# Kernel optimization log

Measured on AMD Instinct MI355X. Metric: run time of the kernel, lower is better.

Reference implementation:

```python
import jax, jax.numpy as jnp
import numpy as np

D = 32        # dmodel (forced by reshape(..., 32) in the original)
N = 2000      # n_nodes == liner_fourth
SLOPE = 0.2   # LeakyReLU negative slope
EPS = 1e-6    # SublayerConnection LayerNorm eps (annotated-transformer style)


def _layernorm(x, g, b):
    m = x.mean(-1, keepdims=True)
    v = x.var(-1, keepdims=True)
    return g * (x - m) / jnp.sqrt(v + EPS) + b


def setup_inputs() -> dict:
    key = jax.random.key(0)
    ks = jax.random.split(key, 18)
    F_, NL, NS = 16, 500, 1500
    s = 0.1
    return {
        "state": jax.random.normal(ks[0], (F_, NS, D), jnp.float32),
        "left": jax.random.normal(ks[1], (F_, NL, D), jnp.float32),
        "inputad": jax.random.bernoulli(ks[2], 0.02, (F_, N, N)).astype(jnp.float32),
        "w3": s * jax.random.normal(ks[3], (D, D), jnp.float32),       # linearThird
        "b3": jnp.zeros((D,), jnp.float32),
        "attn_w": s * jax.random.normal(ks[4], (1, 2 * D), jnp.float32),  # attn (no bias)
        "w4": s * jax.random.normal(ks[5], (D, N), jnp.float32),       # linearFourth: 2000->32
        "b4": jnp.zeros((D,), jnp.float32),
        "w1": s * jax.random.normal(ks[6], (D, D), jnp.float32),       # linear
        "b1": jnp.zeros((D,), jnp.float32),
        "w_ih": s * jax.random.normal(ks[7], (4 * D, D), jnp.float32),  # LSTMCell (gate order i,f,g,o)
        "w_hh": s * jax.random.normal(ks[8], (4 * D, D), jnp.float32),
        "b_ih": jnp.zeros((4 * D,), jnp.float32),
        "b_hh": jnp.zeros((4 * D,), jnp.float32),
        "ln_g": jnp.ones((D,), jnp.float32),                            # SublayerConnection norm
        "ln_b": jnp.zeros((D,), jnp.float32),
        "w2": s * jax.random.normal(ks[9], (D, D), jnp.float32),        # linearSecond
        "b2": jnp.zeros((D,), jnp.float32),
    }


def reference(state, left, inputad, w3, b3, attn_w, w4, b4, w1, b1,
              w_ih, w_hh, b_ih, b_hh, ln_g, ln_b, w2, b2):
    # eval mode: all dropouts are identity
    x = jnp.concatenate([left, state], axis=1)          # [F, N, D]
    F_, n = x.shape[0], x.shape[1]
    g = x @ w3.T + b3                                   # [F, N, D]

    # torch: e = leaky(attn(cat([g.repeat_interleave(n,0), g.repeat(n,1,1)], -1)))
    # Decompose the linear over the concat: attn_w = [a_l | a_r].
    # g_repeat_interleave row m -> g[m // n]; g_repeat row m -> g[m % F_];
    # e.view(F_, n, n)[b, i, j] = e_flat[b*n + i, j].
    a_l, a_r = attn_w[0, :D], attn_w[0, D:]
    s_l = g @ a_l                                        # [F, N]
    s_r = g @ a_r                                        # [F, N]
    idx = (jnp.arange(F_)[:, None] * n + jnp.arange(n)[None, :]) % F_  # [F, N]
    e_mat = jax.nn.leaky_relu(s_l[:, None, :] + s_r[idx], SLOPE)       # [F, N, N]

    e_masked = jnp.where(inputad == 0, 0.0, e_mat)       # masked_fill(adj==0, 0)
    h = jax.nn.leaky_relu(jnp.einsum('bij,oj->bio', e_masked, w4) + b4, SLOPE)  # [F, N, 32]

    # first softmax(e)/dropout pair is dead code (overwritten); a = softmax(h, dim=1)
    a = jax.nn.softmax(h, axis=1)
    st = (a * g) @ w1.T + b1                             # elementwise branch (a.shape == g.shape)

    agg = jnp.matmul(inputad, st)                        # bmm(degree2, state): [F, N, D]

    # SublayerConnection: st + dropout(sublayer(norm(st))); sublayer = LSTMCell cell-state
    nx = _layernorm(st, ln_g, ln_b)
    c0 = nx.reshape(-1, D)                               # initial cell state = norm(st)
    # h0 = zeros, so the w_hh @ h0 contribution vanishes (b_hh still applies)
    gates = agg.reshape(-1, D) @ w_ih.T + b_ih + b_hh    # [F*N, 4D]
    i_g = jax.nn.sigmoid(gates[:, :D])
    f_g = jax.nn.sigmoid(gates[:, D:2 * D])
    g_g = jnp.tanh(gates[:, 2 * D:3 * D])
    c1 = f_g * c0 + i_g * g_g                            # LSTMCell returns (h', c'); [1] -> c'

    out = st + c1.reshape(F_, n, D)
    return out @ w2.T + b2
```

## Files before the change

### kernel.cpp

```cpp
#include <hip/hip_runtime.h>
#include <math.h>

#define F_    16
#define NROW  2000
#define NL    500
#define D     32
#define ROWS  (F_*NROW)
#define SLOPE 0.2f
#define CAP   128
#define LCAP  256

typedef float f4 __attribute__((ext_vector_type(4)));

__global__ __launch_bounds__(256) void k1_g(
    const float* __restrict__ state, const float* __restrict__ left,
    const float* __restrict__ w3, const float* __restrict__ b3,
    const float* __restrict__ attn_w, const float* __restrict__ w4,
    float* __restrict__ g, float* __restrict__ s_l, float* __restrict__ s_r,
    float* __restrict__ w4t)
{
    int bid = blockIdx.x;
    int t = threadIdx.x;
    if (bid >= ROWS/8) {
        int k = (bid - ROWS/8) * 256 + t;
        if (k < D * NROW) {
            int o = k / NROW, j = k - o * NROW;
            w4t[j * D + o] = w4[k];
        }
        return;
    }
    __shared__ float sw3[D*33];
    __shared__ float sb3[D], sal[D], sar[D];
    for (int k = t; k < D*D; k += 256) sw3[(k>>5)*33 + (k&31)] = w3[k];
    if (t < D) { sb3[t] = b3[t]; sal[t] = attn_w[t]; sar[t] = attn_w[D + t]; }
    __syncthreads();
    int grp = t >> 5, lane = t & 31;
    int row = bid * 8 + grp;
    int b = row / NROW, i = row - b * NROW;
    const float* xrow = (i < NL) ? (left  + ((size_t)b * NL + i) * D)
                                 : (state + ((size_t)b * (NROW - NL) + (i - NL)) * D);
    float x = xrow[lane];
    float acc = sb3[lane];
#pragma unroll
    for (int k = 0; k < D; ++k)
        acc += __shfl(x, k, 32) * sw3[lane*33 + k];
    g[(size_t)row * D + lane] = acc;
    float pl = acc * sal[lane], pr = acc * sar[lane];
#pragma unroll
    for (int m = 16; m >= 1; m >>= 1) {
        pl += __shfl_xor(pl, m, 32);
        pr += __shfl_xor(pr, m, 32);
    }
    if (lane == 0) { s_l[row] = pl; s_r[row] = pr; }
}

__global__ __launch_bounds__(256) void k2a_compact(
    const float* __restrict__ adj,
    int* __restrict__ nzc, unsigned short* __restrict__ nzi)
{
    __shared__ unsigned short sh_j[4][LCAP+8];
    int t = threadIdx.x;
    int w = t >> 6, lane = t & 63;
    int row = blockIdx.x * 4 + w;
    const f4* mrow = reinterpret_cast<const f4*>(adj + (size_t)row * NROW);

    f4 v[8];
#pragma unroll
    for (int it = 0; it < 7; ++it)
        v[it] = __builtin_nontemporal_load(mrow + it * 64 + lane);
    v[7] = (f4)(0.f);
    if (448 + lane < NROW/4) v[7] = __builtin_nontemporal_load(mrow + 448 + lane);

    int c = 0;
#pragma unroll
    for (int it = 0; it < 8; ++it)
        c += (v[it][0] != 0.f) + (v[it][1] != 0.f) + (v[it][2] != 0.f) + (v[it][3] != 0.f);
    int inc = c;
#pragma unroll
    for (int off = 1; off < 64; off <<= 1) {
        int n = __shfl_up(inc, off, 64);
        inc += (lane >= off) ? n : 0;
    }
    int pos = inc - c;
    int cnt = __shfl(inc, 63, 64);

#pragma unroll
    for (int it = 0; it < 8; ++it) {
        int jb = (it * 64 + lane) * 4;
#pragma unroll
        for (int cc = 0; cc < 4; ++cc) {
            float val = v[it][cc];
            int hit = (val != 0.f);
            int tgt = (hit && pos < LCAP) ? pos : LCAP;
            sh_j[w][tgt] = (unsigned short)(jb + cc);
            pos += hit;
        }
    }
    int cc2 = (cnt < CAP) ? cnt : CAP;
    for (int k = lane; k < cc2; k += 64)
        nzi[(size_t)row * CAP + k] = sh_j[w][k];
    if (lane == 0) nzc[row] = cc2;
}

__global__ __launch_bounds__(256) void k2b_h(
    const float* __restrict__ s_l, const float* __restrict__ s_r,
    const float* __restrict__ w4t, const float* __restrict__ b4,
    const int* __restrict__ nzc, const unsigned short* __restrict__ nzi,
    float* __restrict__ h)
{
    __shared__ float sh_e[8][CAP];
    __shared__ unsigned short sh_jj[8][CAP];
    int t = threadIdx.x;
    int grp = t >> 5, lane = t & 31;
    int row = blockIdx.x * 8 + grp;
    int b = row / NROW, i = row - b * NROW;
    int r = i & 15;
    int cnt = nzc[row];
    const unsigned short* lst = nzi + (size_t)row * CAP;
    const float* slb = s_l + (size_t)b * NROW;
    const float* srr = s_r + (size_t)r * NROW;
    for (int k = lane; k < cnt; k += 32) {
        int j = lst[k];
        sh_jj[grp][k] = (unsigned short)j;
        float e = slb[j] + srr[j];
        sh_e[grp][k] = (e > 0.f) ? e : SLOPE * e;
    }
    float acc = 0.f;
    int k = 0;
    for (; k + 4 <= cnt; k += 4) {
        int j0 = sh_jj[grp][k],   j1 = sh_jj[grp][k+1];
        int j2 = sh_jj[grp][k+2], j3 = sh_jj[grp][k+3];
        float w0 = w4t[j0*D + lane], w1 = w4t[j1*D + lane];
        float w2v = w4t[j2*D + lane], w3v = w4t[j3*D + lane];
        acc += sh_e[grp][k]   * w0 + sh_e[grp][k+1] * w1
             + sh_e[grp][k+2] * w2v + sh_e[grp][k+3] * w3v;
    }
    for (; k < cnt; ++k)
        acc += sh_e[grp][k] * w4t[sh_jj[grp][k]*D + lane];
    float hv = acc + b4[lane];
    h[(size_t)row * D + lane] = (hv > 0.f) ? hv : SLOPE * hv;
}

__global__ __launch_bounds__(256) void k3a_psum(const float* __restrict__ h,
                                                float* __restrict__ psum)
{
    int b = blockIdx.x, slice = blockIdx.y;
    int t = threadIdx.x;
    int o = t & 31, ti = t >> 5;
    int base = slice * 125;
    float s = 0.f;
    for (int i = base + ti; i < base + 125; i += 8)
        s += expf(h[((size_t)b * NROW + i) * D + o]);
    __shared__ float red[8][D];
    red[ti][o] = s;
    __syncthreads();
    if (t < D) {
        float tot = 0.f;
#pragma unroll
        for (int k = 0; k < 8; ++k) tot += red[k][t];
        psum[((size_t)b * 16 + slice) * D + t] = tot;
    }
}

__global__ __launch_bounds__(256) void k3b_st(
    const float* __restrict__ h, const float* __restrict__ g,
    const float* __restrict__ psum,
    const float* __restrict__ w1, const float* __restrict__ b1,
    float* __restrict__ st)
{
    __shared__ float sw1[D*33], sb1[D], ssum[D];
    int t = threadIdx.x;
    int bid = blockIdx.x;
    int b = bid / 250;
    for (int k = t; k < D*D; k += 256) sw1[(k>>5)*33 + (k&31)] = w1[k];
    if (t < D) {
        sb1[t] = b1[t];
        float tot = 0.f;
#pragma unroll
        for (int s = 0; s < 16; ++s) tot += psum[((size_t)b * 16 + s) * D + t];
        ssum[t] = tot;
    }
    __syncthreads();
    int grp = t >> 5, lane = t & 31;
    size_t row = (size_t)bid * 8 + grp;
    float p = (expf(h[row * D + lane]) / ssum[lane]) * g[row * D + lane];
    float acc = sb1[lane];
#pragma unroll
    for (int k = 0; k < D; ++k)
        acc += __shfl(p, k, 32) * sw1[lane*33 + k];
    st[row * D + lane] = acc;
}

__global__ __launch_bounds__(256) void k4_final(
    const float* __restrict__ st,
    const int* __restrict__ nzc, const unsigned short* __restrict__ nzi,
    const float* __restrict__ w_ih, const float* __restrict__ b_ih,
    const float* __restrict__ b_hh,
    const float* __restrict__ ln_g, const float* __restrict__ ln_b,
    const float* __restrict__ w2, const float* __restrict__ b2,
    float* __restrict__ out)
{
    __shared__ float swih[96*33];
    __shared__ float sw2[D*33];
    __shared__ float sbg[96];
    __shared__ float sb2[D], slg[D], slb[D];
    __shared__ unsigned short jl[8][CAP];
    __shared__ float aggsh[8][D];
    __shared__ float s2sh[8][D];

    int t = threadIdx.x;
    for (int k = t; k < 96*D; k += 256) swih[(k/D)*33 + (k%D)] = w_ih[k];
    for (int k = t; k < D*D;  k += 256) sw2 [(k/D)*33 + (k%D)] = w2[k];
    if (t < 96) sbg[t] = b_ih[t] + b_hh[t];
    if (t < D) { sb2[t] = b2[t]; slg[t] = ln_g[t]; slb[t] = ln_b[t]; }

    int grp = t >> 5, lane = t & 31;
    int row = blockIdx.x * 8 + grp;
    int b = row / NROW;
    int cnt = nzc[row];
    const unsigned short* lst = nzi + (size_t)row * CAP;
    for (int k = lane; k < cnt; k += 32) jl[grp][k] = lst[k];
    __syncthreads();

    const float* stb = st + (size_t)b * NROW * D;
    float agg = 0.f;
    int k = 0;
    for (; k + 8 <= cnt; k += 8) {
        int j0 = jl[grp][k],   j1 = jl[grp][k+1], j2 = jl[grp][k+2], j3 = jl[grp][k+3];
        int j4 = jl[grp][k+4], j5 = jl[grp][k+5], j6 = jl[grp][k+6], j7 = jl[grp][k+7];
        float a0 = stb[j0*D + lane], a1 = stb[j1*D + lane];
        float a2 = stb[j2*D + lane], a3 = stb[j3*D + lane];
        float a4 = stb[j4*D + lane], a5 = stb[j5*D + lane];
        float a6 = stb[j6*D + lane], a7 = stb[j7*D + lane];
        agg += ((a0 + a1) + (a2 + a3)) + ((a4 + a5) + (a6 + a7));
    }
    for (; k < cnt; ++k) agg += stb[jl[grp][k]*D + lane];

    float sv = st[(size_t)row * D + lane];

    float sum = sv;
#pragma unroll
    for (int m = 16; m >= 1; m >>= 1) sum += __shfl_xor(sum, m, 32);
    float mean = sum * (1.f / D);
    float dd = sv - mean;
    float vs = dd * dd;
#pragma unroll
    for (int m = 16; m >= 1; m >>= 1) vs += __shfl_xor(vs, m, 32);
    float inv = 1.f / sqrtf(vs * (1.f / D) + 1e-6f);
    float nx = slg[lane] * dd * inv + slb[lane];

    aggsh[grp][lane] = agg;

    float gi = sbg[lane], gf = sbg[lane + 32], gg = sbg[lane + 64];
#pragma unroll
    for (int d = 0; d < D; ++d) {
        float a = aggsh[grp][d];
        gi += swih[lane*33 + d]      * a;
        gf += swih[(lane+32)*33 + d] * a;
        gg += swih[(lane+64)*33 + d] * a;
    }
    float ig  = 1.f / (1.f + expf(-gi));
    float fg  = 1.f / (1.f + expf(-gf));
    float g_g = tanhf(gg);
    float s2  = sv + fg * nx + ig * g_g;

    s2sh[grp][lane] = s2;

    float acc = sb2[lane];
#pragma unroll
    for (int q = 0; q < D; ++q) acc += sw2[lane*33 + q] * s2sh[grp][q];
    out[(size_t)row * D + lane] = acc;
}

extern "C" void kernel_launch(void* const* d_in, const int* in_sizes, int n_in,
                              void* d_out, int out_size, void* d_ws, size_t ws_size,
                              hipStream_t stream)
{
    const float* state  = (const float*)d_in[0];
    const float* left   = (const float*)d_in[1];
    const float* adj    = (const float*)d_in[2];
    const float* w3     = (const float*)d_in[3];
    const float* b3     = (const float*)d_in[4];
    const float* attn_w = (const float*)d_in[5];
    const float* w4     = (const float*)d_in[6];
    const float* b4     = (const float*)d_in[7];
    const float* w1     = (const float*)d_in[8];
    const float* b1     = (const float*)d_in[9];
    const float* w_ih   = (const float*)d_in[10];
    const float* b_ih   = (const float*)d_in[12];
    const float* b_hh   = (const float*)d_in[13];
    const float* ln_g   = (const float*)d_in[14];
    const float* ln_b   = (const float*)d_in[15];
    const float* w2     = (const float*)d_in[16];
    const float* b2     = (const float*)d_in[17];
    float* out = (float*)d_out;

    float* g    = (float*)d_ws;
    float* h    = g  + (size_t)ROWS * D;
    float* st   = h  + (size_t)ROWS * D;
    float* s_l  = st + (size_t)ROWS * D;
    float* s_r  = s_l + ROWS;
    float* w4t  = s_r + ROWS;
    float* psum = w4t + (size_t)NROW * D;
    int*   nzc  = (int*)(psum + F_ * 16 * D);
    unsigned short* nzi = (unsigned short*)(nzc + ROWS);

    k1_g    <<<dim3(ROWS/8 + (D*NROW+255)/256), dim3(256), 0, stream>>>(
                state, left, w3, b3, attn_w, w4, g, s_l, s_r, w4t);
    k2a_compact<<<dim3(ROWS/4), dim3(256), 0, stream>>>(adj, nzc, nzi);
    k2b_h   <<<dim3(ROWS/8),  dim3(256), 0, stream>>>(s_l, s_r, w4t, b4, nzc, nzi, h);
    k3a_psum<<<dim3(F_, 16),  dim3(256), 0, stream>>>(h, psum);
    k3b_st  <<<dim3(ROWS/8),  dim3(256), 0, stream>>>(h, g, psum, w1, b1, st);
    k4_final<<<dim3(ROWS/8),  dim3(256), 0, stream>>>(st, nzc, nzi, w_ih, b_ih, b_hh,
                                                      ln_g, ln_b, w2, b2, out);
}
```

Before: 132.8 us.

## Fuse six kernels into one persistent kernel with software grid barriers

Replaces the six separate launches with a single persistent kernel of 512 blocks. Each block owns a contiguous slice of rows within one batch, and the phases are separated by atomic-counter grid barriers. The barrier counter is cleared by a memset before the launch. The softmax partial sums are now folded into the h phase, which removes a separate launch. This is meant to remove launch gaps and the small psum kernel, at the cost of having far fewer blocks per phase and relying on every block being co-resident, which could deadlock if not all blocks fit.

```diff
diff --git a/kernel.cpp b/kernel.cpp
--- a/kernel.cpp
+++ b/kernel.cpp
@@ -9,267 +9,266 @@
 #define SLOPE 0.2f
 #define CAP   128
 #define LCAP  256
+#define NBLK  512
+#define TPB   256
 
 typedef float f4 __attribute__((ext_vector_type(4)));
 
-__global__ __launch_bounds__(256) void k1_g(
+struct PA { float sw3[D*33]; float sb3[D]; float sal[D]; float sar[D];
+            unsigned short shj[4][LCAP+8]; };
+struct PB { float red[8][D]; float she[8][CAP]; unsigned short shjj[8][CAP]; };
+struct PC { float sw1[D*33]; float sb1[D]; float ssum[D]; };
+struct PD { float swih[96*33]; float sw2[D*33]; float sbg[96];
+            float sb2[D]; float slg[D]; float slb[D];
+            unsigned short jl[8][CAP]; float aggsh[8][D]; float s2sh[8][D]; };
+union SMU { PA a; PB b; PC c; PD d; };
+
+__device__ __forceinline__ void gridbar(int* bar, int id) {
+    __syncthreads();
+    __threadfence();
+    if (threadIdx.x == 0) {
+        __hip_atomic_fetch_add(bar + id * 32, 1, __ATOMIC_ACQ_REL,
+                               __HIP_MEMORY_SCOPE_AGENT);
+        while (__hip_atomic_load(bar + id * 32, __ATOMIC_ACQUIRE,
+                                 __HIP_MEMORY_SCOPE_AGENT) < NBLK)
+            __builtin_amdgcn_s_sleep(2);
+    }
+    __syncthreads();
+    __threadfence();
+}
+
+__global__ __launch_bounds__(TPB, 2) void mega(
     const float* __restrict__ state, const float* __restrict__ left,
+    const float* __restrict__ adj,
     const float* __restrict__ w3, const float* __restrict__ b3,
     const float* __restrict__ attn_w, const float* __restrict__ w4,
-    float* __restrict__ g, float* __restrict__ s_l, float* __restrict__ s_r,
-    float* __restrict__ w4t)
-{
-    int bid = blockIdx.x;
-    int t = threadIdx.x;
-    if (bid >= ROWS/8) {
-        int k = (bid - ROWS/8) * 256 + t;
-        if (k < D * NROW) {
-            int o = k / NROW, j = k - o * NROW;
-            w4t[j * D + o] = w4[k];
-        }
-        return;
-    }
-    __shared__ float sw3[D*33];
-    __shared__ float sb3[D], sal[D], sar[D];
-    for (int k = t; k < D*D; k += 256) sw3[(k>>5)*33 + (k&31)] = w3[k];
-    if (t < D) { sb3[t] = b3[t]; sal[t] = attn_w[t]; sar[t] = attn_w[D + t]; }
-    __syncthreads();
-    int grp = t >> 5, lane = t & 31;
-    int row = bid * 8 + grp;
-    int b = row / NROW, i = row - b * NROW;
-    const float* xrow = (i < NL) ? (left  + ((size_t)b * NL + i) * D)
-                                 : (state + ((size_t)b * (NROW - NL) + (i - NL)) * D);
-    float x = xrow[lane];
-    float acc = sb3[lane];
-#pragma unroll
-    for (int k = 0; k < D; ++k)
-        acc += __shfl(x, k, 32) * sw3[lane*33 + k];
-    g[(size_t)row * D + lane] = acc;
-    float pl = acc * sal[lane], pr = acc * sar[lane];
-#pragma unroll
-    for (int m = 16; m >= 1; m >>= 1) {
-        pl += __shfl_xor(pl, m, 32);
-        pr += __shfl_xor(pr, m, 32);
-    }
-    if (lane == 0) { s_l[row] = pl; s_r[row] = pr; }
-}
-
-__global__ __launch_bounds__(256) void k2a_compact(
-    const float* __restrict__ adj,
-    int* __restrict__ nzc, unsigned short* __restrict__ nzi)
-{
-    __shared__ unsigned short sh_j[4][LCAP+8];
-    int t = threadIdx.x;
-    int w = t >> 6, lane = t & 63;
-    int row = blockIdx.x * 4 + w;
-    const f4* mrow = reinterpret_cast<const f4*>(adj + (size_t)row * NROW);
-
-    f4 v[8];
-#pragma unroll
-    for (int it = 0; it < 7; ++it)
-        v[it] = __builtin_nontemporal_load(mrow + it * 64 + lane);
-    v[7] = (f4)(0.f);
-    if (448 + lane < NROW/4) v[7] = __builtin_nontemporal_load(mrow + 448 + lane);
-
-    int c = 0;
-#pragma unroll
-    for (int it = 0; it < 8; ++it)
-        c += (v[it][0] != 0.f) + (v[it][1] != 0.f) + (v[it][2] != 0.f) + (v[it][3] != 0.f);
-    int inc = c;
-#pragma unroll
-    for (int off = 1; off < 64; off <<= 1) {
-        int n = __shfl_up(inc, off, 64);
-        inc += (lane >= off) ? n : 0;
-    }
-    int pos = inc - c;
-    int cnt = __shfl(inc, 63, 64);
-
-#pragma unroll
-    for (int it = 0; it < 8; ++it) {
-        int jb = (it * 64 + lane) * 4;
-#pragma unroll
-        for (int cc = 0; cc < 4; ++cc) {
-            float val = v[it][cc];
-            int hit = (val != 0.f);
-            int tgt = (hit && pos < LCAP) ? pos : LCAP;
-            sh_j[w][tgt] = (unsigned short)(jb + cc);
-            pos += hit;
-        }
-    }
-    int cc2 = (cnt < CAP) ? cnt : CAP;
-    for (int k = lane; k < cc2; k += 64)
-        nzi[(size_t)row * CAP + k] = sh_j[w][k];
-    if (lane == 0) nzc[row] = cc2;
-}
-
-__global__ __launch_bounds__(256) void k2b_h(
-    const float* __restrict__ s_l, const float* __restrict__ s_r,
-    const float* __restrict__ w4t, const float* __restrict__ b4,
-    const int* __restrict__ nzc, const unsigned short* __restrict__ nzi,
-    float* __restrict__ h)
-{
-    __shared__ float sh_e[8][CAP];
-    __shared__ unsigned short sh_jj[8][CAP];
-    int t = threadIdx.x;
-    int grp = t >> 5, lane = t & 31;
-    int row = blockIdx.x * 8 + grp;
-    int b = row / NROW, i = row - b * NROW;
-    int r = i & 15;
-    int cnt = nzc[row];
-    const unsigned short* lst = nzi + (size_t)row * CAP;
-    const float* slb = s_l + (size_t)b * NROW;
-    const float* srr = s_r + (size_t)r * NROW;
-    for (int k = lane; k < cnt; k += 32) {
-        int j = lst[k];
-        sh_jj[grp][k] = (unsigned short)j;
-        float e = slb[j] + srr[j];
-        sh_e[grp][k] = (e > 0.f) ? e : SLOPE * e;
-    }
-    float acc = 0.f;
-    int k = 0;
-    for (; k + 4 <= cnt; k += 4) {
-        int j0 = sh_jj[grp][k],   j1 = sh_jj[grp][k+1];
-        int j2 = sh_jj[grp][k+2], j3 = sh_jj[grp][k+3];
-        float w0 = w4t[j0*D + lane], w1 = w4t[j1*D + lane];
-        float w2v = w4t[j2*D + lane], w3v = w4t[j3*D + lane];
-        acc += sh_e[grp][k]   * w0 + sh_e[grp][k+1] * w1
-             + sh_e[grp][k+2] * w2v + sh_e[grp][k+3] * w3v;
-    }
-    for (; k < cnt; ++k)
-        acc += sh_e[grp][k] * w4t[sh_jj[grp][k]*D + lane];
-    float hv = acc + b4[lane];
-    h[(size_t)row * D + lane] = (hv > 0.f) ? hv : SLOPE * hv;
-}
-
-__global__ __launch_bounds__(256) void k3a_psum(const float* __restrict__ h,
-                                                float* __restrict__ psum)
-{
-    int b = blockIdx.x, slice = blockIdx.y;
-    int t = threadIdx.x;
-    int o = t & 31, ti = t >> 5;
-    int base = slice * 125;
-    float s = 0.f;
-    for (int i = base + ti; i < base + 125; i += 8)
-        s += expf(h[((size_t)b * NROW + i) * D + o]);
-    __shared__ float red[8][D];
-    red[ti][o] = s;
-    __syncthreads();
-    if (t < D) {
-        float tot = 0.f;
-#pragma unroll
-        for (int k = 0; k < 8; ++k) tot += red[k][t];
-        psum[((size_t)b * 16 + slice) * D + t] = tot;
-    }
-}
-
-__global__ __launch_bounds__(256) void k3b_st(
-    const float* __restrict__ h, const float* __restrict__ g,
-    const float* __restrict__ psum,
+    const float* __restrict__ b4,
     const float* __restrict__ w1, const float* __restrict__ b1,
-    float* __restrict__ st)
-{
-    __shared__ float sw1[D*33], sb1[D], ssum[D];
-    int t = threadIdx.x;
-    int bid = blockIdx.x;
-    int b = bid / 250;
-    for (int k = t; k < D*D; k += 256) sw1[(k>>5)*33 + (k&31)] = w1[k];
-    if (t < D) {
-        sb1[t] = b1[t];
-        float tot = 0.f;
-#pragma unroll
-        for (int s = 0; s < 16; ++s) tot += psum[((size_t)b * 16 + s) * D + t];
-        ssum[t] = tot;
-    }
-    __syncthreads();
-    int grp = t >> 5, lane = t & 31;
-    size_t row = (size_t)bid * 8 + grp;
-    float p = (expf(h[row * D + lane]) / ssum[lane]) * g[row * D + lane];
-    float acc = sb1[lane];
-#pragma unroll
-    for (int k = 0; k < D; ++k)
-        acc += __shfl(p, k, 32) * sw1[lane*33 + k];
-    st[row * D + lane] = acc;
-}
-
-__global__ __launch_bounds__(256) void k4_final(
-    const float* __restrict__ st,
-    const int* __restrict__ nzc, const unsigned short* __restrict__ nzi,
     const float* __restrict__ w_ih, const float* __restrict__ b_ih,
     const float* __restrict__ b_hh,
     const float* __restrict__ ln_g, const float* __restrict__ ln_b,
     const float* __restrict__ w2, const float* __restrict__ b2,
-    float* __restrict__ out)
+    float* __restrict__ out,
+    int* bar, float* g, float* h, float* st, float* s_l, float* s_r,
+    float* w4t, float* psum, int* nzc, unsigned short* nzi)
 {
-    __shared__ float swih[96*33];
-    __shared__ float sw2[D*33];
-    __shared__ float sbg[96];
-    __shared__ float sb2[D], slg[D], slb[D];
-    __shared__ unsigned short jl[8][CAP];
-    __shared__ float aggsh[8][D];
-    __shared__ float s2sh[8][D];
-
+    __shared__ SMU sm;
+    int q = blockIdx.x;
     int t = threadIdx.x;
-    for (int k = t; k < 96*D; k += 256) swih[(k/D)*33 + (k%D)] = w_ih[k];
-    for (int k = t; k < D*D;  k += 256) sw2 [(k/D)*33 + (k%D)] = w2[k];
-    if (t < 96) sbg[t] = b_ih[t] + b_hh[t];
-    if (t < D) { sb2[t] = b2[t]; slg[t] = ln_g[t]; slb[t] = ln_b[t]; }
-
     int grp = t >> 5, lane = t & 31;
-    int row = blockIdx.x * 8 + grp;
-    int b = row / NROW;
-    int cnt = nzc[row];
-    const unsigned short* lst = nzi + (size_t)row * CAP;
-    for (int k = lane; k < cnt; k += 32) jl[grp][k] = lst[k];
+    int wv = t >> 6, lane64 = t & 63;
+
+    int b  = q >> 5, ss = q & 31;
+    int lo = (ss < 16) ? ss * 63 : 16 * 63 + (ss - 16) * 62;
+    int n  = (ss < 16) ? 63 : 62;
+    int rowbase = b * NROW + lo;
+
+    for (int k = t; k < D*D; k += TPB) sm.a.sw3[(k>>5)*33 + (k&31)] = w3[k];
+    if (t < D) { sm.a.sb3[t] = b3[t]; sm.a.sal[t] = attn_w[t]; sm.a.sar[t] = attn_w[D+t]; }
+    __syncthreads();
+
+    for (int it = 0; it < 8; ++it) {
+        int r = it * 8 + grp;
+        if (r < n) {
+            int row = rowbase + r;
+            int i = lo + r;
+            const float* xrow = (i < NL) ? (left  + ((size_t)b * NL + i) * D)
+                                         : (state + ((size_t)b * (NROW-NL) + (i-NL)) * D);
+            float x = xrow[lane];
+            float acc = sm.a.sb3[lane];
+#pragma unroll
+            for (int k = 0; k < D; ++k)
+                acc += __shfl(x, k, 32) * sm.a.sw3[lane*33 + k];
+            g[(size_t)row * D + lane] = acc;
+            float pl = acc * sm.a.sal[lane], pr = acc * sm.a.sar[lane];
+#pragma unroll
+            for (int m = 16; m >= 1; m >>= 1) {
+                pl += __shfl_xor(pl, m, 32);
+                pr += __shfl_xor(pr, m, 32);
+            }
+            if (lane == 0) { s_l[row] = pl; s_r[row] = pr; }
+        }
+    }
+
+    { int k = q * TPB + t;
+      if (k < D * NROW) { int o = k / NROW, j = k - o * NROW; w4t[j*D + o] = w4[k]; } }
+
+    unsigned long long lmask = (1ull << lane64) - 1ull;
+    for (int rr = wv; rr < n; rr += 4) {
+        int row = rowbase + rr;
+        const f4* mrow = reinterpret_cast<const f4*>(adj + (size_t)row * NROW);
+        f4 v[8];
+#pragma unroll
+        for (int it = 0; it < 7; ++it)
+            v[it] = __builtin_nontemporal_load(mrow + it * 64 + lane64);
+        v[7] = (f4)(0.f);
+        if (448 + lane64 < NROW/4) v[7] = __builtin_nontemporal_load(mrow + 448 + lane64);
+
+        int c = 0;
+#pragma unroll
+        for (int it = 0; it < 8; ++it)
+            c += (v[it][0]!=0.f) + (v[it][1]!=0.f) + (v[it][2]!=0.f) + (v[it][3]!=0.f);
+        int inc = c;
+#pragma unroll
+        for (int off = 1; off < 64; off <<= 1) {
+            int nn = __shfl_up(inc, off, 64);
+            inc += (lane64 >= off) ? nn : 0;
+        }
+        int pos = inc - c;
+        int cnt = __shfl(inc, 63, 64);
+#pragma unroll
+        for (int it = 0; it < 8; ++it) {
+            int jb = (it * 64 + lane64) * 4;
+#pragma unroll
+            for (int cc = 0; cc < 4; ++cc) {
+                int hit = (v[it][cc] != 0.f);
+                int tgt = (hit && pos < LCAP) ? pos : LCAP;
+                sm.a.shj[wv][tgt] = (unsigned short)(jb + cc);
+                pos += hit;
+            }
+        }
+        int cc2 = (cnt < CAP) ? cnt : CAP;
+        for (int k = lane64; k < cc2; k += 64)
+            nzi[(size_t)row * CAP + k] = sm.a.shj[wv][k];
+        if (lane64 == 0) nzc[row] = cc2;
+    }
+
+    gridbar(bar, 0);
+
+    float esum = 0.f;
+    for (int it = 0; it < 8; ++it) {
+        int r = it * 8 + grp;
+        if (r < n) {
+            int row = rowbase + r;
+            int i = lo + r;
+            int cnt = nzc[row];
+            const unsigned short* lst = nzi + (size_t)row * CAP;
+            const float* slb = s_l + (size_t)b * NROW;
+            const float* srr = s_r + (size_t)(i & 15) * NROW;
+            for (int k = lane; k < cnt; k += 32) {
+                int j = lst[k];
+                sm.b.shjj[grp][k] = (unsigned short)j;
+                float e = slb[j] + srr[j];
+                sm.b.she[grp][k] = (e > 0.f) ? e : SLOPE * e;
+            }
+            float acc = 0.f;
+            int k = 0;
+            for (; k + 4 <= cnt; k += 4) {
+                int j0 = sm.b.shjj[grp][k],   j1 = sm.b.shjj[grp][k+1];
+                int j2 = sm.b.shjj[grp][k+2], j3 = sm.b.shjj[grp][k+3];
+                acc += sm.b.she[grp][k]   * w4t[j0*D + lane]
+                     + sm.b.she[grp][k+1] * w4t[j1*D + lane]
+                     + sm.b.she[grp][k+2] * w4t[j2*D + lane]
+                     + sm.b.she[grp][k+3] * w4t[j3*D + lane];
+            }
+            for (; k < cnt; ++k)
+                acc += sm.b.she[grp][k] * w4t[sm.b.shjj[grp][k]*D + lane];
+            float hv = acc + b4[lane];
+            hv = (hv > 0.f) ? hv : SLOPE * hv;
+            h[(size_t)row * D + lane] = hv;
+            esum += expf(hv);
+        }
+    }
+    sm.b.red[grp][lane] = esum;
+    __syncthreads();
+    if (t < D) {
+        float tot = 0.f;
+#pragma unroll
+        for (int k = 0; k < 8; ++k) tot += sm.b.red[k][t];
+        psum[q * D + t] = tot;
+    }
+
+    gridbar(bar, 1);
+
+    for (int k = t; k < D*D; k += TPB) sm.c.sw1[(k>>5)*33 + (k&31)] = w1[k];
+    if (t < D) {
+        sm.c.sb1[t] = b1[t];
+        float tot = 0.f;
+#pragma unroll
+        for (int s = 0; s < 32; ++s) tot += psum[(b * 32 + s) * D + t];
+        sm.c.ssum[t] = tot;
+    }
+    __syncthreads();
+    for (int it = 0; it < 8; ++it) {
+        int r = it * 8 + grp;
+        if (r < n) {
+            size_t row = (size_t)rowbase + r;
+            float p = (expf(h[row*D + lane]) / sm.c.ssum[lane]) * g[row*D + lane];
+            float acc = sm.c.sb1[lane];
+#pragma unroll
+            for (int k = 0; k < D; ++k)
+                acc += __shfl(p, k, 32) * sm.c.sw1[lane*33 + k];
+            st[row*D + lane] = acc;
+        }
+    }
+
+    gridbar(bar, 2);
+
+    for (int k = t; k < 96*D; k += TPB) sm.d.swih[(k/D)*33 + (k%D)] = w_ih[k];
+    for (int k = t; k < D*D;  k += TPB) sm.d.sw2 [(k/D)*33 + (k%D)] = w2[k];
+    if (t < 96) sm.d.sbg[t] = b_ih[t] + b_hh[t];
+    if (t < D) { sm.d.sb2[t] = b2[t]; sm.d.slg[t] = ln_g[t]; sm.d.slb[t] = ln_b[t]; }
     __syncthreads();
 
     const float* stb = st + (size_t)b * NROW * D;
-    float agg = 0.f;
-    int k = 0;
-    for (; k + 8 <= cnt; k += 8) {
-        int j0 = jl[grp][k],   j1 = jl[grp][k+1], j2 = jl[grp][k+2], j3 = jl[grp][k+3];
-        int j4 = jl[grp][k+4], j5 = jl[grp][k+5], j6 = jl[grp][k+6], j7 = jl[grp][k+7];
-        float a0 = stb[j0*D + lane], a1 = stb[j1*D + lane];
-        float a2 = stb[j2*D + lane], a3 = stb[j3*D + lane];
-        float a4 = stb[j4*D + lane], a5 = stb[j5*D + lane];
-        float a6 = stb[j6*D + lane], a7 = stb[j7*D + lane];
-        agg += ((a0 + a1) + (a2 + a3)) + ((a4 + a5) + (a6 + a7));
-    }
-    for (; k < cnt; ++k) agg += stb[jl[grp][k]*D + lane];
-
-    float sv = st[(size_t)row * D + lane];
-
-    float sum = sv;
-#pragma unroll
-    for (int m = 16; m >= 1; m >>= 1) sum += __shfl_xor(sum, m, 32);
-    float mean = sum * (1.f / D);
-    float dd = sv - mean;
-    float vs = dd * dd;
-#pragma unroll
-    for (int m = 16; m >= 1; m >>= 1) vs += __shfl_xor(vs, m, 32);
-    float inv = 1.f / sqrtf(vs * (1.f / D) + 1e-6f);
-    float nx = slg[lane] * dd * inv + slb[lane];
-
-    aggsh[grp][lane] = agg;
-
-    float gi = sbg[lane], gf = sbg[lane + 32], gg = sbg[lane + 64];
-#pragma unroll
-    for (int d = 0; d < D; ++d) {
-        float a = aggsh[grp][d];
-        gi += swih[lane*33 + d]      * a;
-        gf += swih[(lane+32)*33 + d] * a;
-        gg += swih[(lane+64)*33 + d] * a;
-    }
-    float ig  = 1.f / (1.f + expf(-gi));
-    float fg  = 1.f / (1.f + expf(-gf));
-    float g_g = tanhf(gg);
-    float s2  = sv + fg * nx + ig * g_g;
-
-    s2sh[grp][lane] = s2;
-
-    float acc = sb2[lane];
-#pragma unroll
-    for (int q = 0; q < D; ++q) acc += sw2[lane*33 + q] * s2sh[grp][q];
-    out[(size_t)row * D + lane] = acc;
+    for (int it = 0; it < 8; ++it) {
+        int r = it * 8 + grp;
+        if (r < n) {
+            int row = rowbase + r;
+            int cnt = nzc[row];
+            const unsigned short* lst = nzi + (size_t)row * CAP;
+            for (int k = lane; k < cnt; k += 32) sm.d.jl[grp][k] = lst[k];
+
+            float agg = 0.f;
+            int k = 0;
+            for (; k + 8 <= cnt; k += 8) {
+                int j0 = sm.d.jl[grp][k],   j1 = sm.d.jl[grp][k+1];
+                int j2 = sm.d.jl[grp][k+2], j3 = sm.d.jl[grp][k+3];
+                int j4 = sm.d.jl[grp][k+4], j5 = sm.d.jl[grp][k+5];
+                int j6 = sm.d.jl[grp][k+6], j7 = sm.d.jl[grp][k+7];
+                float a0 = stb[j0*D + lane], a1 = stb[j1*D + lane];
+                float a2 = stb[j2*D + lane], a3 = stb[j3*D + lane];
+                float a4 = stb[j4*D + lane], a5 = stb[j5*D + lane];
+                float a6 = stb[j6*D + lane], a7 = stb[j7*D + lane];
+                agg += ((a0+a1) + (a2+a3)) + ((a4+a5) + (a6+a7));
+            }
+            for (; k < cnt; ++k) agg += stb[sm.d.jl[grp][k]*D + lane];
+
+            float sv = st[(size_t)row * D + lane];
+            float sum = sv;
+#pragma unroll
+            for (int m = 16; m >= 1; m >>= 1) sum += __shfl_xor(sum, m, 32);
+            float mean = sum * (1.f / D);
+            float dd = sv - mean;
+            float vs = dd * dd;
+#pragma unroll
+            for (int m = 16; m >= 1; m >>= 1) vs += __shfl_xor(vs, m, 32);
+            float inv = 1.f / sqrtf(vs * (1.f / D) + 1e-6f);
+            float nx = sm.d.slg[lane] * dd * inv + sm.d.slb[lane];
+
+            sm.d.aggsh[grp][lane] = agg;
+
+            float gi = sm.d.sbg[lane], gf = sm.d.sbg[lane+32], gg = sm.d.sbg[lane+64];
+#pragma unroll
+            for (int d = 0; d < D; ++d) {
+                float a = sm.d.aggsh[grp][d];
+                gi += sm.d.swih[lane*33 + d]      * a;
+                gf += sm.d.swih[(lane+32)*33 + d] * a;
+                gg += sm.d.swih[(lane+64)*33 + d] * a;
+            }
+            float ig  = 1.f / (1.f + expf(-gi));
+            float fg  = 1.f / (1.f + expf(-gf));
+            float g_g = tanhf(gg);
+            float s2  = sv + fg * nx + ig * g_g;
+
+            sm.d.s2sh[grp][lane] = s2;
+
+            float acc = sm.d.sb2[lane];
+#pragma unroll
+            for (int qq = 0; qq < D; ++qq) acc += sm.d.sw2[lane*33 + qq] * sm.d.s2sh[grp][qq];
+            out[(size_t)row * D + lane] = acc;
+        }
+    }
 }
 
 extern "C" void kernel_launch(void* const* d_in, const int* in_sizes, int n_in,
@@ -295,22 +294,20 @@
     const float* b2     = (const float*)d_in[17];
     float* out = (float*)d_out;
 
-    float* g    = (float*)d_ws;
+    int*   bar  = (int*)d_ws;
+    float* g    = (float*)((char*)d_ws + 1024);
     float* h    = g  + (size_t)ROWS * D;
     float* st   = h  + (size_t)ROWS * D;
     float* s_l  = st + (size_t)ROWS * D;
     float* s_r  = s_l + ROWS;
     float* w4t  = s_r + ROWS;
     float* psum = w4t + (size_t)NROW * D;
-    int*   nzc  = (int*)(psum + F_ * 16 * D);
+    int*   nzc  = (int*)(psum + NBLK * D);
     unsigned short* nzi = (unsigned short*)(nzc + ROWS);
 
-    k1_g    <<<dim3(ROWS/8 + (D*NROW+255)/256), dim3(256), 0, stream>>>(
-                state, left, w3, b3, attn_w, w4, g, s_l, s_r, w4t);
-    k2a_compact<<<dim3(ROWS/4), dim3(256), 0, stream>>>(adj, nzc, nzi);
-    k2b_h   <<<dim3(ROWS/8),  dim3(256), 0, stream>>>(s_l, s_r, w4t, b4, nzc, nzi, h);
-    k3a_psum<<<dim3(F_, 16),  dim3(256), 0, stream>>>(h, psum);
-    k3b_st  <<<dim3(ROWS/8),  dim3(256), 0, stream>>>(h, g, psum, w1, b1, st);
-    k4_final<<<dim3(ROWS/8),  dim3(256), 0, stream>>>(st, nzc, nzi, w_ih, b_ih, b_hh,
-                                                      ln_g, ln_b, w2, b2, out);
+    hipMemsetAsync(bar, 0, 1024, stream);
+    mega<<<dim3(NBLK), dim3(TPB), 0, stream>>>(
+        state, left, adj, w3, b3, attn_w, w4, b4, w1, b1,
+        w_ih, b_ih, b_hh, ln_g, ln_b, w2, b2, out,
+        bar, g, h, st, s_l, s_r, w4t, psum, nzc, nzi);
 }
```

Result: slower. 521.5 us (+292.9%).

## Flatten adjacency compaction into grid-stride stream with atomics; fuse softmax sums

Applied to the files above, without the earlier changes.

Replaces the one-row-per-wave compaction of the dense adjacency with a flat grid-stride stream over the whole matrix. Each wave builds per-row prefix sums from ballots and reserves slots with atomicAdd on per-row counters, which are zeroed by a memset. The per-column exp-sum for the softmax is folded into the h kernel through atomic adds, which removes the separate partial-sum kernel. Neighbour order and summation order become nondeterministic, and each step now pays for atomics and scattered narrow stores.

```diff
diff --git a/kernel.cpp b/kernel.cpp
--- a/kernel.cpp
+++ b/kernel.cpp
@@ -8,7 +8,9 @@
 #define ROWS  (F_*NROW)
 #define SLOPE 0.2f
 #define CAP   128
-#define LCAP  256
+#define NF4   (ROWS*NROW/4)
+#define SBLK  2048
+#define STRD  (SBLK*256)
 
 typedef float f4 __attribute__((ext_vector_type(4)));
 
@@ -54,68 +56,65 @@
     if (lane == 0) { s_l[row] = pl; s_r[row] = pr; }
 }
 
-__global__ __launch_bounds__(256) void k2a_compact(
+__global__ __launch_bounds__(256) void k2a_flat(
     const float* __restrict__ adj,
     int* __restrict__ nzc, unsigned short* __restrict__ nzi)
 {
-    __shared__ unsigned short sh_j[4][LCAP+8];
-    int t = threadIdx.x;
-    int w = t >> 6, lane = t & 63;
-    int row = blockIdx.x * 4 + w;
-    const f4* mrow = reinterpret_cast<const f4*>(adj + (size_t)row * NROW);
-
-    f4 v[8];
-#pragma unroll
-    for (int it = 0; it < 7; ++it)
-        v[it] = __builtin_nontemporal_load(mrow + it * 64 + lane);
-    v[7] = (f4)(0.f);
-    if (448 + lane < NROW/4) v[7] = __builtin_nontemporal_load(mrow + 448 + lane);
-
-    int c = 0;
-#pragma unroll
-    for (int it = 0; it < 8; ++it)
-        c += (v[it][0] != 0.f) + (v[it][1] != 0.f) + (v[it][2] != 0.f) + (v[it][3] != 0.f);
-    int inc = c;
-#pragma unroll
-    for (int off = 1; off < 64; off <<= 1) {
-        int n = __shfl_up(inc, off, 64);
-        inc += (lane >= off) ? n : 0;
-    }
-    int pos = inc - c;
-    int cnt = __shfl(inc, 63, 64);
-
-#pragma unroll
-    for (int it = 0; it < 8; ++it) {
-        int jb = (it * 64 + lane) * 4;
-#pragma unroll
-        for (int cc = 0; cc < 4; ++cc) {
-            float val = v[it][cc];
-            int hit = (val != 0.f);
-            int tgt = (hit && pos < LCAP) ? pos : LCAP;
-            sh_j[w][tgt] = (unsigned short)(jb + cc);
-            pos += hit;
-        }
-    }
-    int cc2 = (cnt < CAP) ? cnt : CAP;
-    for (int k = lane; k < cc2; k += 64)
-        nzi[(size_t)row * CAP + k] = sh_j[w][k];
-    if (lane == 0) nzc[row] = cc2;
+    const f4* adj4 = reinterpret_cast<const f4*>(adj);
+    int tid = blockIdx.x * 256 + threadIdx.x;
+    int lane = threadIdx.x & 63;
+    unsigned long long lmask = (1ull << lane) - 1ull;
+
+    for (int idx = tid; idx < NF4; idx += STRD) {
+        f4 v = adj4[idx];
+        int row = idx / 500;
+        int jb  = (idx - row * 500) * 4;
+        int h0 = (v[0] != 0.f), h1 = (v[1] != 0.f);
+        int h2 = (v[2] != 0.f), h3 = (v[3] != 0.f);
+        int nh = h0 + h1 + h2 + h3;
+
+        int row0 = __shfl(row, 0, 64);
+        unsigned long long g0 = __ballot(row == row0);
+        unsigned long long act = __ballot(1);
+        unsigned long long same = (row == row0) ? g0 : (act & ~g0);
+
+        unsigned long long p0 = __ballot(nh & 1);
+        unsigned long long p1 = __ballot(nh & 2);
+        unsigned long long p2 = __ballot(nh & 4);
+        unsigned long long pm = same & lmask;
+        int prefix = __popcll(p0 & pm) + 2*__popcll(p1 & pm) + 4*__popcll(p2 & pm);
+        int total  = __popcll(p0 & same) + 2*__popcll(p1 & same) + 4*__popcll(p2 & same);
+
+        int lead = (int)__builtin_ctzll(same);
+        int base = 0;
+        if (lane == lead && total > 0)
+            base = atomicAdd(&nzc[row], total);
+        base = __shfl(base, lead, 64);
+
+        int slot = base + prefix;
+        unsigned short* nrow = nzi + (size_t)row * CAP;
+        if (h0) { if (slot < CAP) nrow[slot] = (unsigned short)(jb);     slot++; }
+        if (h1) { if (slot < CAP) nrow[slot] = (unsigned short)(jb + 1); slot++; }
+        if (h2) { if (slot < CAP) nrow[slot] = (unsigned short)(jb + 2); slot++; }
+        if (h3) { if (slot < CAP) nrow[slot] = (unsigned short)(jb + 3); slot++; }
+    }
 }
 
 __global__ __launch_bounds__(256) void k2b_h(
     const float* __restrict__ s_l, const float* __restrict__ s_r,
     const float* __restrict__ w4t, const float* __restrict__ b4,
     const int* __restrict__ nzc, const unsigned short* __restrict__ nzi,
-    float* __restrict__ h)
+    float* __restrict__ h, float* __restrict__ psum)
 {
     __shared__ float sh_e[8][CAP];
     __shared__ unsigned short sh_jj[8][CAP];
+    __shared__ float red[8][D];
     int t = threadIdx.x;
     int grp = t >> 5, lane = t & 31;
     int row = blockIdx.x * 8 + grp;
     int b = row / NROW, i = row - b * NROW;
     int r = i & 15;
-    int cnt = nzc[row];
+    int cnt = nzc[row]; cnt = (cnt < CAP) ? cnt : CAP;
     const unsigned short* lst = nzi + (size_t)row * CAP;
     const float* slb = s_l + (size_t)b * NROW;
     const float* srr = s_r + (size_t)r * NROW;
@@ -130,35 +129,21 @@
     for (; k + 4 <= cnt; k += 4) {
         int j0 = sh_jj[grp][k],   j1 = sh_jj[grp][k+1];
         int j2 = sh_jj[grp][k+2], j3 = sh_jj[grp][k+3];
-        float w0 = w4t[j0*D + lane], w1 = w4t[j1*D + lane];
-        float w2v = w4t[j2*D + lane], w3v = w4t[j3*D + lane];
-        acc += sh_e[grp][k]   * w0 + sh_e[grp][k+1] * w1
-             + sh_e[grp][k+2] * w2v + sh_e[grp][k+3] * w3v;
+        acc += sh_e[grp][k]   * w4t[j0*D + lane] + sh_e[grp][k+1] * w4t[j1*D + lane]
+             + sh_e[grp][k+2] * w4t[j2*D + lane] + sh_e[grp][k+3] * w4t[j3*D + lane];
     }
     for (; k < cnt; ++k)
         acc += sh_e[grp][k] * w4t[sh_jj[grp][k]*D + lane];
     float hv = acc + b4[lane];
-    h[(size_t)row * D + lane] = (hv > 0.f) ? hv : SLOPE * hv;
-}
-
-__global__ __launch_bounds__(256) void k3a_psum(const float* __restrict__ h,
-                                                float* __restrict__ psum)
-{
-    int b = blockIdx.x, slice = blockIdx.y;
-    int t = threadIdx.x;
-    int o = t & 31, ti = t >> 5;
-    int base = slice * 125;
-    float s = 0.f;
-    for (int i = base + ti; i < base + 125; i += 8)
-        s += expf(h[((size_t)b * NROW + i) * D + o]);
-    __shared__ float red[8][D];
-    red[ti][o] = s;
+    hv = (hv > 0.f) ? hv : SLOPE * hv;
+    h[(size_t)row * D + lane] = hv;
+    red[grp][lane] = expf(hv);
     __syncthreads();
     if (t < D) {
         float tot = 0.f;
 #pragma unroll
-        for (int k = 0; k < 8; ++k) tot += red[k][t];
-        psum[((size_t)b * 16 + slice) * D + t] = tot;
+        for (int kk = 0; kk < 8; ++kk) tot += red[kk][t];
+        atomicAdd(&psum[b * D + t], tot);
     }
 }
 
@@ -173,13 +158,7 @@
     int bid = blockIdx.x;
     int b = bid / 250;
     for (int k = t; k < D*D; k += 256) sw1[(k>>5)*33 + (k&31)] = w1[k];
-    if (t < D) {
-        sb1[t] = b1[t];
-        float tot = 0.f;
-#pragma unroll
-        for (int s = 0; s < 16; ++s) tot += psum[((size_t)b * 16 + s) * D + t];
-        ssum[t] = tot;
-    }
+    if (t < D) { sb1[t] = b1[t]; ssum[t] = psum[b * D + t]; }
     __syncthreads();
     int grp = t >> 5, lane = t & 31;
     size_t row = (size_t)bid * 8 + grp;
@@ -217,7 +196,7 @@
     int grp = t >> 5, lane = t & 31;
     int row = blockIdx.x * 8 + grp;
     int b = row / NROW;
-    int cnt = nzc[row];
+    int cnt = nzc[row]; cnt = (cnt < CAP) ? cnt : CAP;
     const unsigned short* lst = nzi + (size_t)row * CAP;
     for (int k = lane; k < cnt; k += 32) jl[grp][k] = lst[k];
     __syncthreads();
@@ -301,15 +280,16 @@
     float* s_l  = st + (size_t)ROWS * D;
     float* s_r  = s_l + ROWS;
     float* w4t  = s_r + ROWS;
-    float* psum = w4t + (size_t)NROW * D;
-    int*   nzc  = (int*)(psum + F_ * 16 * D);
-    unsigned short* nzi = (unsigned short*)(nzc + ROWS);
+    int*   nzc  = (int*)(w4t + (size_t)NROW * D);
+    float* psum = (float*)(nzc + ROWS);
+    unsigned short* nzi = (unsigned short*)(psum + F_ * D);
+
+    hipMemsetAsync(nzc, 0, ROWS * sizeof(int) + F_ * D * sizeof(float), stream);
 
     k1_g    <<<dim3(ROWS/8 + (D*NROW+255)/256), dim3(256), 0, stream>>>(
                 state, left, w3, b3, attn_w, w4, g, s_l, s_r, w4t);
-    k2a_compact<<<dim3(ROWS/4), dim3(256), 0, stream>>>(adj, nzc, nzi);
-    k2b_h   <<<dim3(ROWS/8),  dim3(256), 0, stream>>>(s_l, s_r, w4t, b4, nzc, nzi, h);
-    k3a_psum<<<dim3(F_, 16),  dim3(256), 0, stream>>>(h, psum);
+    k2a_flat<<<dim3(SBLK),    dim3(256), 0, stream>>>(adj, nzc, nzi);
+    k2b_h   <<<dim3(ROWS/8),  dim3(256), 0, stream>>>(s_l, s_r, w4t, b4, nzc, nzi, h, psum);
     k3b_st  <<<dim3(ROWS/8),  dim3(256), 0, stream>>>(h, g, psum, w1, b1, st);
     k4_final<<<dim3(ROWS/8),  dim3(256), 0, stream>>>(st, nzc, nzi, w_ih, b_ih, b_hh,
                                                       ln_g, ln_b, w2, b2, out);
```

After: 154.9 us. 1.17x slower.

## Store adjacency as bitmask and fuse softmax column sums into h kernel

Applied to the files above, without the earlier changes.

The compaction kernel now writes a per-row 2000-bit mask instead of a capped index list. Each consumer kernel (h and final aggregation) rebuilds the neighbour list from the mask with popcount, a prefix scan and ctz loops. The separate psum kernel is removed: the h kernel reduces exp(h) per block and atomically adds into a zeroed per-batch sum. This drops a launch and cuts intermediate traffic, at the cost of decoding the mask twice, float atomics that make the summation order nondeterministic, and an extra memset.

```diff
diff --git a/kernel.cpp b/kernel.cpp
--- a/kernel.cpp
+++ b/kernel.cpp
@@ -8,7 +8,6 @@
 #define ROWS  (F_*NROW)
 #define SLOPE 0.2f
 #define CAP   128
-#define LCAP  256
 
 typedef float f4 __attribute__((ext_vector_type(4)));
 
@@ -54,111 +53,103 @@
     if (lane == 0) { s_l[row] = pl; s_r[row] = pr; }
 }
 
-__global__ __launch_bounds__(256) void k2a_compact(
-    const float* __restrict__ adj,
-    int* __restrict__ nzc, unsigned short* __restrict__ nzi)
-{
-    __shared__ unsigned short sh_j[4][LCAP+8];
+__global__ __launch_bounds__(256) void k2_bits(
+    const float* __restrict__ adj, unsigned* __restrict__ nzm)
+{
     int t = threadIdx.x;
     int w = t >> 6, lane = t & 63;
     int row = blockIdx.x * 4 + w;
     const f4* mrow = reinterpret_cast<const f4*>(adj + (size_t)row * NROW);
-
     f4 v[8];
 #pragma unroll
     for (int it = 0; it < 7; ++it)
-        v[it] = __builtin_nontemporal_load(mrow + it * 64 + lane);
+        v[it] = mrow[it * 64 + lane];
     v[7] = (f4)(0.f);
-    if (448 + lane < NROW/4) v[7] = __builtin_nontemporal_load(mrow + 448 + lane);
-
-    int c = 0;
-#pragma unroll
-    for (int it = 0; it < 8; ++it)
-        c += (v[it][0] != 0.f) + (v[it][1] != 0.f) + (v[it][2] != 0.f) + (v[it][3] != 0.f);
+    if (448 + lane < NROW/4) v[7] = mrow[448 + lane];
+    unsigned m = 0u;
+#pragma unroll
+    for (int it = 0; it < 8; ++it) {
+        m |= (v[it][0] != 0.f ? 1u : 0u) << (it*4);
+        m |= (v[it][1] != 0.f ? 1u : 0u) << (it*4+1);
+        m |= (v[it][2] != 0.f ? 1u : 0u) << (it*4+2);
+        m |= (v[it][3] != 0.f ? 1u : 0u) << (it*4+3);
+    }
+    nzm[(size_t)row * 64 + lane] = m;
+}
+
+__device__ __forceinline__ int bits_to_list(
+    const unsigned* __restrict__ wrow, int lane,
+    unsigned short* __restrict__ jl )
+{
+    unsigned wr0 = wrow[lane], wr1 = wrow[32 + lane];
+    int c = __popc(wr0) + __popc(wr1);
     int inc = c;
 #pragma unroll
-    for (int off = 1; off < 64; off <<= 1) {
-        int n = __shfl_up(inc, off, 64);
+    for (int off = 1; off < 32; off <<= 1) {
+        int n = __shfl_up(inc, off, 32);
         inc += (lane >= off) ? n : 0;
     }
     int pos = inc - c;
-    int cnt = __shfl(inc, 63, 64);
-
-#pragma unroll
-    for (int it = 0; it < 8; ++it) {
-        int jb = (it * 64 + lane) * 4;
-#pragma unroll
-        for (int cc = 0; cc < 4; ++cc) {
-            float val = v[it][cc];
-            int hit = (val != 0.f);
-            int tgt = (hit && pos < LCAP) ? pos : LCAP;
-            sh_j[w][tgt] = (unsigned short)(jb + cc);
-            pos += hit;
-        }
-    }
-    int cc2 = (cnt < CAP) ? cnt : CAP;
-    for (int k = lane; k < cc2; k += 64)
-        nzi[(size_t)row * CAP + k] = sh_j[w][k];
-    if (lane == 0) nzc[row] = cc2;
+    int cnt = __shfl(inc, 31, 32);
+    cnt = (cnt < CAP) ? cnt : CAP;
+    unsigned m = wr0; int wb = lane * 4;
+    while (m) {
+        int b = __builtin_ctz(m); m &= m - 1;
+        if (pos < CAP) jl[pos] = (unsigned short)((b >> 2) * 256 + wb + (b & 3));
+        ++pos;
+    }
+    m = wr1; wb = (32 + lane) * 4;
+    while (m) {
+        int b = __builtin_ctz(m); m &= m - 1;
+        if (pos < CAP) jl[pos] = (unsigned short)((b >> 2) * 256 + wb + (b & 3));
+        ++pos;
+    }
+    return cnt;
 }
 
 __global__ __launch_bounds__(256) void k2b_h(
     const float* __restrict__ s_l, const float* __restrict__ s_r,
     const float* __restrict__ w4t, const float* __restrict__ b4,
-    const int* __restrict__ nzc, const unsigned short* __restrict__ nzi,
-    float* __restrict__ h)
-{
-    __shared__ float sh_e[8][CAP];
-    __shared__ unsigned short sh_jj[8][CAP];
+    const unsigned* __restrict__ nzm,
+    float* __restrict__ h, float* __restrict__ psum)
+{
+    __shared__ unsigned short jl[8][CAP];
+    __shared__ float she[8][CAP];
+    __shared__ float red[8][D];
     int t = threadIdx.x;
     int grp = t >> 5, lane = t & 31;
     int row = blockIdx.x * 8 + grp;
     int b = row / NROW, i = row - b * NROW;
     int r = i & 15;
-    int cnt = nzc[row];
-    const unsigned short* lst = nzi + (size_t)row * CAP;
+    int cnt = bits_to_list(nzm + (size_t)row * 64, lane, jl[grp]);
+
     const float* slb = s_l + (size_t)b * NROW;
     const float* srr = s_r + (size_t)r * NROW;
     for (int k = lane; k < cnt; k += 32) {
-        int j = lst[k];
-        sh_jj[grp][k] = (unsigned short)j;
+        int j = jl[grp][k];
         float e = slb[j] + srr[j];
-        sh_e[grp][k] = (e > 0.f) ? e : SLOPE * e;
+        she[grp][k] = (e > 0.f) ? e : SLOPE * e;
     }
     float acc = 0.f;
     int k = 0;
     for (; k + 4 <= cnt; k += 4) {
-        int j0 = sh_jj[grp][k],   j1 = sh_jj[grp][k+1];
-        int j2 = sh_jj[grp][k+2], j3 = sh_jj[grp][k+3];
-        float w0 = w4t[j0*D + lane], w1 = w4t[j1*D + lane];
-        float w2v = w4t[j2*D + lane], w3v = w4t[j3*D + lane];
-        acc += sh_e[grp][k]   * w0 + sh_e[grp][k+1] * w1
-             + sh_e[grp][k+2] * w2v + sh_e[grp][k+3] * w3v;
+        int j0 = jl[grp][k],   j1 = jl[grp][k+1];
+        int j2 = jl[grp][k+2], j3 = jl[grp][k+3];
+        acc += she[grp][k]   * w4t[j0*D + lane] + she[grp][k+1] * w4t[j1*D + lane]
+             + she[grp][k+2] * w4t[j2*D + lane] + she[grp][k+3] * w4t[j3*D + lane];
     }
     for (; k < cnt; ++k)
-        acc += sh_e[grp][k] * w4t[sh_jj[grp][k]*D + lane];
+        acc += she[grp][k] * w4t[jl[grp][k]*D + lane];
     float hv = acc + b4[lane];
-    h[(size_t)row * D + lane] = (hv > 0.f) ? hv : SLOPE * hv;
-}
-
-__global__ __launch_bounds__(256) void k3a_psum(const float* __restrict__ h,
-                                                float* __restrict__ psum)
-{
-    int b = blockIdx.x, slice = blockIdx.y;
-    int t = threadIdx.x;
-    int o = t & 31, ti = t >> 5;
-    int base = slice * 125;
-    float s = 0.f;
-    for (int i = base + ti; i < base + 125; i += 8)
-        s += expf(h[((size_t)b * NROW + i) * D + o]);
-    __shared__ float red[8][D];
-    red[ti][o] = s;
+    hv = (hv > 0.f) ? hv : SLOPE * hv;
+    h[(size_t)row * D + lane] = hv;
+    red[grp][lane] = expf(hv);
     __syncthreads();
     if (t < D) {
         float tot = 0.f;
 #pragma unroll
-        for (int k = 0; k < 8; ++k) tot += red[k][t];
-        psum[((size_t)b * 16 + slice) * D + t] = tot;
+        for (int kk = 0; kk < 8; ++kk) tot += red[kk][t];
+        atomicAdd(&psum[b * D + t], tot);
     }
 }
 
@@ -173,13 +164,7 @@
     int bid = blockIdx.x;
     int b = bid / 250;
     for (int k = t; k < D*D; k += 256) sw1[(k>>5)*33 + (k&31)] = w1[k];
-    if (t < D) {
-        sb1[t] = b1[t];
-        float tot = 0.f;
-#pragma unroll
-        for (int s = 0; s < 16; ++s) tot += psum[((size_t)b * 16 + s) * D + t];
-        ssum[t] = tot;
-    }
+    if (t < D) { sb1[t] = b1[t]; ssum[t] = psum[b * D + t]; }
     __syncthreads();
     int grp = t >> 5, lane = t & 31;
     size_t row = (size_t)bid * 8 + grp;
@@ -192,8 +177,7 @@
 }
 
 __global__ __launch_bounds__(256) void k4_final(
-    const float* __restrict__ st,
-    const int* __restrict__ nzc, const unsigned short* __restrict__ nzi,
+    const float* __restrict__ st, const unsigned* __restrict__ nzm,
     const float* __restrict__ w_ih, const float* __restrict__ b_ih,
     const float* __restrict__ b_hh,
     const float* __restrict__ ln_g, const float* __restrict__ ln_b,
@@ -217,9 +201,7 @@
     int grp = t >> 5, lane = t & 31;
     int row = blockIdx.x * 8 + grp;
     int b = row / NROW;
-    int cnt = nzc[row];
-    const unsigned short* lst = nzi + (size_t)row * CAP;
-    for (int k = lane; k < cnt; k += 32) jl[grp][k] = lst[k];
+    int cnt = bits_to_list(nzm + (size_t)row * 64, lane, jl[grp]);
     __syncthreads();
 
     const float* stb = st + (size_t)b * NROW * D;
@@ -302,15 +284,15 @@
     float* s_r  = s_l + ROWS;
     float* w4t  = s_r + ROWS;
     float* psum = w4t + (size_t)NROW * D;
-    int*   nzc  = (int*)(psum + F_ * 16 * D);
-    unsigned short* nzi = (unsigned short*)(nzc + ROWS);
-
-    k1_g    <<<dim3(ROWS/8 + (D*NROW+255)/256), dim3(256), 0, stream>>>(
-                state, left, w3, b3, attn_w, w4, g, s_l, s_r, w4t);
-    k2a_compact<<<dim3(ROWS/4), dim3(256), 0, stream>>>(adj, nzc, nzi);
-    k2b_h   <<<dim3(ROWS/8),  dim3(256), 0, stream>>>(s_l, s_r, w4t, b4, nzc, nzi, h);
-    k3a_psum<<<dim3(F_, 16),  dim3(256), 0, stream>>>(h, psum);
-    k3b_st  <<<dim3(ROWS/8),  dim3(256), 0, stream>>>(h, g, psum, w1, b1, st);
-    k4_final<<<dim3(ROWS/8),  dim3(256), 0, stream>>>(st, nzc, nzi, w_ih, b_ih, b_hh,
-                                                      ln_g, ln_b, w2, b2, out);
-}
+    unsigned* nzm = (unsigned*)(psum + F_ * D);
+
+    hipMemsetAsync(psum, 0, F_ * D * sizeof(float), stream);
+
+    k1_g   <<<dim3(ROWS/8 + (D*NROW+255)/256), dim3(256), 0, stream>>>(
+               state, left, w3, b3, attn_w, w4, g, s_l, s_r, w4t);
+    k2_bits<<<dim3(ROWS/4),  dim3(256), 0, stream>>>(adj, nzm);
+    k2b_h  <<<dim3(ROWS/8),  dim3(256), 0, stream>>>(s_l, s_r, w4t, b4, nzm, h, psum);
+    k3b_st <<<dim3(ROWS/8),  dim3(256), 0, stream>>>(h, g, psum, w1, b1, st);
+    k4_final<<<dim3(ROWS/8), dim3(256), 0, stream>>>(st, nzm, w_ih, b_ih, b_hh,
+                                                     ln_g, ln_b, w2, b2, out);
+}
```

New measurement: 140.4 us. 5.8% more time.
